# Kernel tuning notes

Hardware: AMD Instinct MI355X
Metric: run time of the kernel (lower is better)

Reference implementation:

```python
import jax, jax.numpy as jnp
import numpy as np

NEG_SLOPE = 0.2  # PyG GATConv default leaky_relu slope


def gat_conv(x, ei, W, a_src, a_dst, b, heads, ch):
    """One PyG-style GATConv (eval mode, add_self_loops already applied to ei)."""
    N = x.shape[0]
    h = (x @ W).reshape(N, heads, ch)                      # [N,H,C]
    src, dst = ei[0], ei[1]
    al_s = jnp.sum(h * a_src, axis=-1)                     # [N,H]
    al_d = jnp.sum(h * a_dst, axis=-1)                     # [N,H]
    e = jax.nn.leaky_relu(al_s[src] + al_d[dst], NEG_SLOPE)  # [E,H]
    m = jax.ops.segment_max(e, dst, num_segments=N)        # stable softmax over in-edges
    ex = jnp.exp(e - m[dst])
    den = jax.ops.segment_sum(ex, dst, num_segments=N)
    alpha = ex / den[dst]                                  # [E,H]
    msg = alpha[:, :, None] * h[src]                       # [E,H,C]
    out = jax.ops.segment_sum(msg, dst, num_segments=N)    # [N,H,C]
    return out.reshape(N, heads * ch) + b


def setup_inputs() -> dict:
    key = jax.random.key(0)
    ks = jax.random.split(key, 12)
    N, E, D_in, C, H, D_out = 10000, 320000, 256, 128, 4, 64
    HC = H * C

    def glorot(k, shape):
        fan = shape[0] + shape[-1]
        return jax.random.normal(k, shape, dtype=jnp.float32) * np.sqrt(2.0 / fan)

    x = jax.random.normal(ks[0], (N, D_in), dtype=jnp.float32)
    edge_index = jax.random.randint(ks[1], (2, E), 0, N, dtype=jnp.int64)
    return {
        "x": x,
        "edge_index": edge_index,
        "W1": glorot(ks[2], (D_in, HC)),
        "a_src1": glorot(ks[3], (H, C)),
        "a_dst1": glorot(ks[4], (H, C)),
        "b1": jnp.zeros((HC,), dtype=jnp.float32),
        "W2": glorot(ks[5], (HC, HC)),
        "a_src2": glorot(ks[6], (H, C)),
        "a_dst2": glorot(ks[7], (H, C)),
        "b2": jnp.zeros((HC,), dtype=jnp.float32),
        "W3": glorot(ks[8], (HC, D_out)),
        "a_src3": glorot(ks[9], (1, D_out)),
        "a_dst3": glorot(ks[10], (1, D_out)),
        "b3": jnp.zeros((D_out,), dtype=jnp.float32),
    }


def reference(x, edge_index, W1, a_src1, a_dst1, b1, W2, a_src2, a_dst2, b2,
              W3, a_src3, a_dst3, b3):
    N = x.shape[0]
    loops = jnp.arange(N, dtype=edge_index.dtype)
    ei = jnp.concatenate([edge_index, jnp.stack([loops, loops])], axis=1)
    H, C = a_src1.shape
    h = jax.nn.elu(gat_conv(x, ei, W1, a_src1, a_dst1, b1, H, C))
    h = jax.nn.elu(gat_conv(h, ei, W2, a_src2, a_dst2, b2, H, C))
    out = gat_conv(h, ei, W3, a_src3, a_dst3, b3, 1, a_src3.shape[1])
    return out
```

## Files before the change

kernel.cpp:

```cpp
#include <hip/hip_runtime.h>
#include <hip/hip_fp16.h>

typedef _Float16 f16x8 __attribute__((ext_vector_type(8)));
typedef float f32x4 __attribute__((ext_vector_type(4)));

__device__ __forceinline__ unsigned short f2h_bits(float f) {
    __half h = __float2half(f);
    return *reinterpret_cast<unsigned short*>(&h);
}
__device__ __forceinline__ float h2f_bits(unsigned short u) {
    __half h = *reinterpret_cast<__half*>(&u);
    return __half2float(h);
}

__device__ __forceinline__ void fma_mix_lo(float& acc, float a, unsigned hw) {
    asm("v_fma_mix_f32 %0, %1, %2, %0 op_sel_hi:[0,1,0]"
        : "+v"(acc) : "v"(a), "v"(hw));
}
__device__ __forceinline__ void fma_mix_hi(float& acc, float a, unsigned hw) {
    asm("v_fma_mix_f32 %0, %1, %2, %0 op_sel:[0,1,0] op_sel_hi:[0,1,0]"
        : "+v"(acc) : "v"(a), "v"(hw));
}

__device__ __forceinline__ void gload_lds16(const void* g, void* l) {
    __builtin_amdgcn_global_load_lds(
        (const __attribute__((address_space(1))) unsigned int*)g,
        (__attribute__((address_space(3))) unsigned int*)l, 16, 0, 0);
}

__global__ void k_prep(const float* __restrict__ W1, unsigned short* __restrict__ W1T,
                       const float* __restrict__ W2, unsigned short* __restrict__ W2T,
                       const float* __restrict__ W3, unsigned short* __restrict__ W3T,
                       const float* __restrict__ x, unsigned short* __restrict__ xb,
                       int* __restrict__ csr, int Mcap,
                       const int* __restrict__ ei, int E, int* __restrict__ deg,
                       int DIN, int HC, int DOUT, int N)
{
    int i = blockIdx.x * blockDim.x + threadIdx.x;
    int n1 = DIN * HC;
    int n2 = n1 + HC * HC;
    int n3 = n2 + HC * DOUT;
    int n4 = n3 + N * DIN;
    int n5 = n4 + Mcap;
    int n6 = n5 + E;
    if (i < n1) {
        int k = i / HC, n = i - k * HC;
        W1T[n * DIN + k] = f2h_bits(W1[i]);
    } else if (i < n2) {
        int j = i - n1;
        int k = j / HC, n = j - k * HC;
        W2T[n * HC + k] = f2h_bits(W2[j]);
    } else if (i < n3) {
        int j = i - n2;
        int k = j / DOUT, n = j - k * DOUT;
        W3T[n * HC + k] = f2h_bits(W3[j]);
    } else if (i < n4) {
        int j = i - n3;
        xb[j] = f2h_bits(x[j]);
    } else if (i < n5) {
        csr[i - n4] = -1;
    } else if (i < n6) {
        atomicAdd(&deg[ei[E + (i - n5)]], 1);
    }
}

__global__ void k_scan(const int* __restrict__ deg, int* __restrict__ off,
                       int* __restrict__ cur, int N) {
    __shared__ int sums[1024];
    int t = threadIdx.x;
    int chunk = (N + 1023) >> 10;
    int lo = t * chunk;
    int hi = lo + chunk; if (hi > N) hi = N;
    if (lo > N) lo = N;
    int s = 0;
    for (int i = lo; i < hi; ++i) s += (deg[i] + 4) & ~3;
    sums[t] = s;
    __syncthreads();
    for (int dd = 1; dd < 1024; dd <<= 1) {
        int v = (t >= dd) ? sums[t - dd] : 0;
        __syncthreads();
        sums[t] += v;
        __syncthreads();
    }
    int run = sums[t] - s;
    for (int i = lo; i < hi; ++i) { off[i] = run; cur[i] = run; run += (deg[i] + 4) & ~3; }
    if (t == 1023) off[N] = run;
}
__global__ void k_fill(const int* __restrict__ ei, int E, int N,
                       int* cur, int* __restrict__ csr, int* __restrict__ dstarr) {
    int i = blockIdx.x * blockDim.x + threadIdx.x;
    if (i < E) {
        int s = ei[i], d = ei[E + i];
        int pos = atomicAdd(&cur[d], 1);
        csr[pos] = s;
        dstarr[pos] = d;
    } else if (i < E + N) {
        int nn = i - E;
        int pos = atomicAdd(&cur[nn], 1);
        csr[pos] = nn;
        dstarr[pos] = nn;
    }
}

template <bool OUTH, bool DOAL>
__global__ __launch_bounds__(256) void k_gemm(
    const unsigned short* __restrict__ A, const unsigned short* __restrict__ BT,
    void* __restrict__ D, int M, int K, int Nc, int tiles_n,
    const float* __restrict__ asrc, const float* __restrict__ adst,
    float* __restrict__ als, float* __restrict__ ald)
{
    int wid = blockIdx.x * (blockDim.x >> 6) + (threadIdx.x >> 6);
    int tiles_m = (M + 63) >> 6;
    if (wid >= tiles_m * tiles_n) return;
    int lane = threadIdx.x & 63;
    int tm = wid / tiles_n, tn = wid - tm * tiles_n;
    int m0 = tm << 6, n0 = tn << 6;
    int r = lane & 15, q = lane >> 4;

    const unsigned short* Arow[4];
    const unsigned short* Brow[4];
#pragma unroll
    for (int i = 0; i < 4; ++i) {
        int row = m0 + 16 * i + r; row = row < M ? row : M - 1;
        Arow[i] = A + (size_t)row * K + q * 8;
        Brow[i] = BT + (size_t)(n0 + 16 * i + r) * K + q * 8;
    }

    f32x4 acc[4][4] = {};
    f16x8 a[4], b[4], a2[4], b2[4];
#pragma unroll
    for (int i = 0; i < 4; ++i) {
        a[i] = *(const f16x8*)(Arow[i]);
        b[i] = *(const f16x8*)(Brow[i]);
    }
    for (int k0 = 0; k0 < K; k0 += 32) {
        int kn = k0 + 32;
        if (kn < K) {
#pragma unroll
            for (int i = 0; i < 4; ++i) {
                a2[i] = *(const f16x8*)(Arow[i] + kn);
                b2[i] = *(const f16x8*)(Brow[i] + kn);
            }
        }
#pragma unroll
        for (int i = 0; i < 4; ++i)
#pragma unroll
            for (int j = 0; j < 4; ++j)
                acc[i][j] = __builtin_amdgcn_mfma_f32_16x16x32_f16(a[i], b[j], acc[i][j], 0, 0, 0);
        if (kn < K) {
#pragma unroll
            for (int i = 0; i < 4; ++i) { a[i] = a2[i]; b[i] = b2[i]; }
        }
    }
#pragma unroll
    for (int i = 0; i < 4; ++i) {
        int rowb = m0 + 16 * i + q * 4;
#pragma unroll
        for (int rr = 0; rr < 4; ++rr) {
            int row = rowb + rr;
            if (row < M) {
#pragma unroll
                for (int j = 0; j < 4; ++j) {
                    int col = n0 + 16 * j + r;
                    if (OUTH)
                        ((unsigned short*)D)[(size_t)row * Nc + col] = f2h_bits(acc[i][j][rr]);
                    else
                        ((float*)D)[(size_t)row * Nc + col] = acc[i][j][rr];
                }
            }
        }
    }
    if (DOAL) {
        float asl[4], adl[4];
#pragma unroll
        for (int j = 0; j < 4; ++j) { asl[j] = asrc[16 * j + r]; adl[j] = adst[16 * j + r]; }
#pragma unroll
        for (int i = 0; i < 4; ++i) {
#pragma unroll
            for (int rr = 0; rr < 4; ++rr) {
                float s = 0.f, d = 0.f;
#pragma unroll
                for (int j = 0; j < 4; ++j) {
                    s += acc[i][j][rr] * asl[j];
                    d += acc[i][j][rr] * adl[j];
                }
#pragma unroll
                for (int dd = 1; dd < 16; dd <<= 1) {
                    s += __shfl_xor(s, dd);
                    d += __shfl_xor(d, dd);
                }
                int row = m0 + 16 * i + q * 4 + rr;
                if (r == 0 && row < M) { als[row] = s; ald[row] = d; }
            }
        }
    }
}

__global__ __launch_bounds__(256) void k_gemm_lds(
    const unsigned short* __restrict__ A, const unsigned short* __restrict__ BT,
    unsigned short* __restrict__ D, int M, int K, int Nc, int tiles_n)
{
    __shared__ unsigned short As[128 * 32];
    __shared__ unsigned short Bs[64 * 32];
    int tm = blockIdx.x / tiles_n, tn = blockIdx.x - tm * tiles_n;
    int m0 = tm << 7, n0 = tn << 6;
    int tid = threadIdx.x;
    int w = tid >> 6, lane = tid & 63;
    int wr = w >> 1, wc = w & 1;
    int r = lane & 15, q = lane >> 4;

    int lrow = lane >> 2;
    int lch = (lane & 3) * 8;
    int ga0 = m0 + w * 16 + lrow;       if (ga0 >= M) ga0 = M - 1;
    int ga1 = m0 + (w + 4) * 16 + lrow; if (ga1 >= M) ga1 = M - 1;
    const unsigned short* pa0 = A + (size_t)ga0 * K + lch;
    const unsigned short* pa1 = A + (size_t)ga1 * K + lch;
    const unsigned short* pb  = BT + (size_t)(n0 + w * 16 + lrow) * K + lch;
    unsigned short* lA0 = As + w * 512;
    unsigned short* lA1 = As + (w + 4) * 512;
    unsigned short* lB  = Bs + w * 512;

    const unsigned short* arp = As + (wr * 64 + r) * 32 + q * 8;
    const unsigned short* brp = Bs + (wc * 32 + r) * 32 + q * 8;

    f32x4 acc[4][2] = {};
    for (int k0 = 0; k0 < K; k0 += 32) {
        gload_lds16(pa0 + k0, lA0);
        gload_lds16(pa1 + k0, lA1);
        gload_lds16(pb + k0, lB);
        __syncthreads();
        f16x8 a[4], b[2];
#pragma unroll
        for (int i = 0; i < 4; ++i) a[i] = *(const f16x8*)(arp + i * 16 * 32);
#pragma unroll
        for (int j = 0; j < 2; ++j) b[j] = *(const f16x8*)(brp + j * 16 * 32);
#pragma unroll
        for (int i = 0; i < 4; ++i)
#pragma unroll
            for (int j = 0; j < 2; ++j)
                acc[i][j] = __builtin_amdgcn_mfma_f32_16x16x32_f16(a[i], b[j], acc[i][j], 0, 0, 0);
        __syncthreads();
    }
#pragma unroll
    for (int i = 0; i < 4; ++i) {
        int rowb = m0 + wr * 64 + 16 * i + q * 4;
#pragma unroll
        for (int rr = 0; rr < 4; ++rr) {
            int row = rowb + rr;
            if (row < M) {
#pragma unroll
                for (int j = 0; j < 2; ++j) {
                    int col = n0 + wc * 32 + 16 * j + r;
                    D[(size_t)row * Nc + col] = f2h_bits(acc[i][j][rr]);
                }
            }
        }
    }
}

template <int HCt, int Ht>
__global__ __launch_bounds__(256) void k_al(
    const unsigned short* __restrict__ h, const float* __restrict__ asrc,
    const float* __restrict__ adst,
    float* __restrict__ als, float* __restrict__ ald, int N)
{
    int wid = blockIdx.x * (blockDim.x >> 6) + (threadIdx.x >> 6);
    if (wid >= N) return;
    int lane = threadIdx.x & 63;
    const int CH = HCt / 64;
    const int Gs = 64 / Ht;
    float s = 0.f, d = 0.f;
    if constexpr (CH == 8) {
        const uint4* hr = (const uint4*)(h + (size_t)wid * HCt) + lane;
        uint4 hv = *hr;
        unsigned wds[4] = {hv.x, hv.y, hv.z, hv.w};
        const f32x4* as4 = (const f32x4*)(asrc + lane * 8);
        const f32x4* ad4 = (const f32x4*)(adst + lane * 8);
        f32x4 av0 = as4[0], av1 = as4[1], dv0 = ad4[0], dv1 = ad4[1];
#pragma unroll
        for (int wv = 0; wv < 4; ++wv) {
            float a0 = (wv < 2) ? av0[2 * wv] : av1[2 * (wv - 2)];
            float a1 = (wv < 2) ? av0[2 * wv + 1] : av1[2 * (wv - 2) + 1];
            float d0 = (wv < 2) ? dv0[2 * wv] : dv1[2 * (wv - 2)];
            float d1 = (wv < 2) ? dv0[2 * wv + 1] : dv1[2 * (wv - 2) + 1];
            fma_mix_lo(s, a0, wds[wv]); fma_mix_hi(s, a1, wds[wv]);
            fma_mix_lo(d, d0, wds[wv]); fma_mix_hi(d, d1, wds[wv]);
        }
    } else {
        float hv = h2f_bits(h[(size_t)wid * HCt + lane]);
        s = hv * asrc[lane];
        d = hv * adst[lane];
    }
#pragma unroll
    for (int dd = 1; dd < Gs; dd <<= 1) {
        s += __shfl_xor(s, dd);
        d += __shfl_xor(d, dd);
    }
    if ((lane & (Gs - 1)) == 0) {
        int hh = lane / Gs;
        als[wid * Ht + hh] = s;
        ald[wid * Ht + hh] = d;
    }
}

__global__ void k_alpha4(const float* __restrict__ als, const float* __restrict__ ald,
                         const int* __restrict__ csr, const int* __restrict__ dstarr,
                         const int* __restrict__ off, int N,
                         float* __restrict__ alpha, int Mcap)
{
    int t = blockIdx.x * blockDim.x + threadIdx.x;
    if (t >= off[N]) return;
    int s = csr[t];
    if (s < 0) {
#pragma unroll
        for (int h = 0; h < 4; ++h) alpha[(size_t)h * Mcap + t] = 0.f;
        return;
    }
    int d = dstarr[t];
    f32x4 a = *(const f32x4*)(als + (size_t)s * 4);
    f32x4 b = *(const f32x4*)(ald + (size_t)d * 4);
#pragma unroll
    for (int h = 0; h < 4; ++h) {
        float l = a[h] + b[h];
        l = l > 0.f ? l : 0.2f * l;
        alpha[(size_t)h * Mcap + t] = __expf(l);
    }
}

template <bool DOELU>
__global__ __launch_bounds__(256) void k_aggr4b(
    const unsigned short* __restrict__ h, const float* __restrict__ alpha,
    const int* __restrict__ off, const int* __restrict__ csr,
    const float* __restrict__ bias,
    unsigned short* __restrict__ outp, int N, int nodeBlocks, int Mcap)
{
    int head = blockIdx.x / nodeBlocks;
    int nb = blockIdx.x - head * nodeBlocks;
    int n = nb * 4 + (threadIdx.x >> 6);
    if (n >= N) return;
    int lane = threadIdx.x & 63;
    int g = lane >> 4;
    int p = lane & 15;
    int q0 = (off[n] >> 2) + g, q1 = off[n + 1] >> 2;

    float acc[8] = {};
    float den = 0.f;
    const char* hB = (const char*)h;
    const unsigned offp = (unsigned)(head * 256 + p * 16);
    const int4* csr4 = (const int4*)csr;
    const f32x4* al4 = (const f32x4*)(alpha + (size_t)head * Mcap);

    auto fmaq = [&](float a, const uint4& hq) {
        unsigned wds[4] = {hq.x, hq.y, hq.z, hq.w};
#pragma unroll
        for (int wv = 0; wv < 4; ++wv) {
            fma_mix_lo(acc[2 * wv],     a, wds[wv]);
            fma_mix_hi(acc[2 * wv + 1], a, wds[wv]);
        }
    };

    for (int q = q0; q < q1; q += 4) {
        int4 cs = csr4[q];
        f32x4 av = al4[q];
        int c0 = cs.x < 0 ? 0 : cs.x;
        int c1 = cs.y < 0 ? 0 : cs.y;
        int c2 = cs.z < 0 ? 0 : cs.z;
        int c3 = cs.w < 0 ? 0 : cs.w;
        uint4 h0 = *(const uint4*)(hB + (size_t)((((unsigned)c0) << 10) + offp));
        uint4 h1 = *(const uint4*)(hB + (size_t)((((unsigned)c1) << 10) + offp));
        uint4 h2 = *(const uint4*)(hB + (size_t)((((unsigned)c2) << 10) + offp));
        uint4 h3 = *(const uint4*)(hB + (size_t)((((unsigned)c3) << 10) + offp));
        den += (av[0] + av[1]) + (av[2] + av[3]);
        fmaq(av[0], h0);
        fmaq(av[1], h1);
        fmaq(av[2], h2);
        fmaq(av[3], h3);
    }

    den += __shfl_xor(den, 16);
    den += __shfl_xor(den, 32);
#pragma unroll
    for (int j = 0; j < 8; ++j) {
        acc[j] += __shfl_xor(acc[j], 16);
        acc[j] += __shfl_xor(acc[j], 32);
    }

    if (g == 0) {
        float inv = 1.f / den;
        int cb = head * 128 + p * 8;
        unsigned ww[4];
#pragma unroll
        for (int wv = 0; wv < 4; ++wv) {
            float v0 = acc[2 * wv] * inv + bias[cb + 2 * wv];
            float v1 = acc[2 * wv + 1] * inv + bias[cb + 2 * wv + 1];
            if (DOELU) {
                v0 = v0 > 0.f ? v0 : expm1f(v0);
                v1 = v1 > 0.f ? v1 : expm1f(v1);
            }
            ww[wv] = (unsigned)f2h_bits(v0) | ((unsigned)f2h_bits(v1) << 16);
        }
        uint4 o; o.x = ww[0]; o.y = ww[1]; o.z = ww[2]; o.w = ww[3];
        *((uint4*)(outp + (size_t)n * 512 + cb)) = o;
    }
}

__global__ __launch_bounds__(256) void k_aggr1b(
    const unsigned short* __restrict__ h, const float* __restrict__ als,
    const float* __restrict__ aldv, const int* __restrict__ off,
    const int* __restrict__ csr, const float* __restrict__ bias,
    float* __restrict__ outp, int N)
{
    int n = blockIdx.x * (blockDim.x >> 6) + (threadIdx.x >> 6);
    if (n >= N) return;
    int lane = threadIdx.x & 63;
    int g = lane >> 4;
    int p = lane & 15;
    int q0 = (off[n] >> 2) + g, q1 = off[n + 1] >> 2;
    float aldh = aldv[n];

    float acc[4] = {};
    float den = 0.f;
    const char* hB = (const char*)h;
    const unsigned offp = (unsigned)(p * 8);
    const int4* csr4 = (const int4*)csr;

    auto aof = [&](int ss) -> float {
        int sc = ss < 0 ? 0 : ss;
        float l = als[sc] + aldh;
        l = l > 0.f ? l : 0.2f * l;
        float e = __expf(l);
        return ss < 0 ? 0.f : e;
    };
    auto fmaq = [&](float a, const uint2& hq) {
        den += a;
        fma_mix_lo(acc[0], a, hq.x);
        fma_mix_hi(acc[1], a, hq.x);
        fma_mix_lo(acc[2], a, hq.y);
        fma_mix_hi(acc[3], a, hq.y);
    };

    for (int q = q0; q < q1; q += 4) {
        int4 cs = csr4[q];
        float a0 = aof(cs.x), a1 = aof(cs.y), a2 = aof(cs.z), a3 = aof(cs.w);
        uint2 h0 = *(const uint2*)(hB + (size_t)((((unsigned)(cs.x < 0 ? 0 : cs.x)) << 7) + offp));
        uint2 h1 = *(const uint2*)(hB + (size_t)((((unsigned)(cs.y < 0 ? 0 : cs.y)) << 7) + offp));
        uint2 h2 = *(const uint2*)(hB + (size_t)((((unsigned)(cs.z < 0 ? 0 : cs.z)) << 7) + offp));
        uint2 h3 = *(const uint2*)(hB + (size_t)((((unsigned)(cs.w < 0 ? 0 : cs.w)) << 7) + offp));
        fmaq(a0, h0);
        fmaq(a1, h1);
        fmaq(a2, h2);
        fmaq(a3, h3);
    }

    den += __shfl_xor(den, 16);
    den += __shfl_xor(den, 32);
#pragma unroll
    for (int j = 0; j < 4; ++j) {
        acc[j] += __shfl_xor(acc[j], 16);
        acc[j] += __shfl_xor(acc[j], 32);
    }
    if (g == 0) {
        float inv = 1.f / den;
        f32x4 o;
#pragma unroll
        for (int j = 0; j < 4; ++j)
            o[j] = acc[j] * inv + bias[p * 4 + j];
        *((f32x4*)(outp + (size_t)n * 64 + p * 4)) = o;
    }
}

extern "C" void kernel_launch(void* const* d_in, const int* in_sizes, int n_in,
                              void* d_out, int out_size, void* d_ws, size_t ws_size,
                              hipStream_t stream)
{
    const float* x   = (const float*)d_in[0];
    const int*   ei  = (const int*)d_in[1];
    const float* W1  = (const float*)d_in[2];
    const float* as1 = (const float*)d_in[3];
    const float* ad1 = (const float*)d_in[4];
    const float* b1  = (const float*)d_in[5];
    const float* W2  = (const float*)d_in[6];
    const float* as2 = (const float*)d_in[7];
    const float* ad2 = (const float*)d_in[8];
    const float* b2  = (const float*)d_in[9];
    const float* W3  = (const float*)d_in[10];
    const float* as3 = (const float*)d_in[11];
    const float* ad3 = (const float*)d_in[12];
    const float* b3  = (const float*)d_in[13];

    const int DIN = 256, HC = 512, DOUT = 64;
    int N = in_sizes[0] / DIN;
    int E = in_sizes[1] / 2;
    int Mcap = E + 4 * N;

    char* w = (char*)d_ws;
    auto alloc = [&](size_t bytes) -> char* {
        char* p = w;
        w += (bytes + 255) & ~(size_t)255;
        return p;
    };
    int* deg    = (int*)alloc((size_t)N * 4);
    int* cur    = (int*)alloc((size_t)N * 4);
    int* off    = (int*)alloc((size_t)(N + 1) * 4);
    int* csr    = (int*)alloc((size_t)Mcap * 4);
    int* dstarr = (int*)alloc((size_t)Mcap * 4);
    unsigned short* W1T = (unsigned short*)alloc((size_t)HC * DIN * 2);
    unsigned short* W2T = (unsigned short*)alloc((size_t)HC * HC * 2);
    unsigned short* W3T = (unsigned short*)alloc((size_t)DOUT * HC * 2);
    unsigned short* xb  = (unsigned short*)alloc((size_t)N * DIN * 2);
    unsigned short* act = (unsigned short*)alloc((size_t)N * HC * 2);
    unsigned short* hb  = (unsigned short*)alloc((size_t)N * HC * 2);
    unsigned short* hb3 = (unsigned short*)alloc((size_t)N * DOUT * 2);
    float* als   = (float*)alloc((size_t)N * 4 * 4);
    float* ald   = (float*)alloc((size_t)N * 4 * 4);
    float* alpha = (float*)alloc((size_t)Mcap * 4 * 4);

    hipMemsetAsync(deg, 0, (size_t)N * 4, stream);
    int prep_total = DIN * HC + HC * HC + HC * DOUT + N * DIN + Mcap + E;
    k_prep<<<(prep_total + 255) / 256, 256, 0, stream>>>(
        W1, W1T, W2, W2T, W3, W3T, x, xb, csr, Mcap, ei, E, deg, DIN, HC, DOUT, N);
    k_scan<<<1, 1024, 0, stream>>>(deg, off, cur, N);
    k_fill<<<(E + N + 255) / 256, 256, 0, stream>>>(ei, E, N, cur, csr, dstarr);

    int tiles_m = (N + 63) / 64;
    auto gemm_blocks = [&](int tn) { return (tiles_m * tn + 3) / 4; };
    int tm128 = (N + 127) / 128;
    int nwave_blocks = (N + 3) / 4;
    int nodeBlocks = (N + 3) / 4;
    int alpha_blocks = (Mcap + 255) / 256;

    k_gemm_lds<<<tm128 * (HC / 64), 256, 0, stream>>>(xb, W1T, hb, N, DIN, HC, HC / 64);
    k_al<512, 4><<<nwave_blocks, 256, 0, stream>>>(hb, as1, ad1, als, ald, N);
    k_alpha4<<<alpha_blocks, 256, 0, stream>>>(als, ald, csr, dstarr, off, N, alpha, Mcap);
    k_aggr4b<true><<<4 * nodeBlocks, 256, 0, stream>>>(hb, alpha, off, csr, b1, act, N, nodeBlocks, Mcap);

    k_gemm_lds<<<tm128 * (HC / 64), 256, 0, stream>>>(act, W2T, hb, N, HC, HC, HC / 64);
    k_al<512, 4><<<nwave_blocks, 256, 0, stream>>>(hb, as2, ad2, als, ald, N);
    k_alpha4<<<alpha_blocks, 256, 0, stream>>>(als, ald, csr, dstarr, off, N, alpha, Mcap);
    k_aggr4b<true><<<4 * nodeBlocks, 256, 0, stream>>>(hb, alpha, off, csr, b2, act, N, nodeBlocks, Mcap);

    k_gemm<true, true><<<gemm_blocks(1), 256, 0, stream>>>(
        act, W3T, hb3, N, HC, DOUT, 1, as3, ad3, als, ald);
    k_aggr1b<<<nwave_blocks, 256, 0, stream>>>(hb3, als, ald, off, csr, b3, (float*)d_out, N);
}
```

Baseline: 286.3 us.

## Fuse attention coefficient computation into aggregation and process all heads per wave

Removes the separate per-edge alpha kernel and its Mcap×4 alpha buffer (and the dstarr array). Each wave now computes exp(leaky_relu(als[src]+ald[dst])) for 64 edges at a time into shared memory, then aggregates all 4 heads per node with each lane covering 8 channels across the full 512-wide row. This saves a kernel launch and a global write-then-read of alpha per layer, and each csr row is read once instead of once per head. In exchange, per-node work is serialized within one wave with a shared-memory staging step, and the launch has 4x fewer blocks.

Measured after the change: 283.9 us. Within noise of the previous version (-0.8%).

```diff
diff --git a/kernel.cpp b/kernel.cpp
--- a/kernel.cpp
+++ b/kernel.cpp
@@ -87,18 +87,16 @@
     if (t == 1023) off[N] = run;
 }
 __global__ void k_fill(const int* __restrict__ ei, int E, int N,
-                       int* cur, int* __restrict__ csr, int* __restrict__ dstarr) {
+                       int* cur, int* __restrict__ csr) {
     int i = blockIdx.x * blockDim.x + threadIdx.x;
     if (i < E) {
         int s = ei[i], d = ei[E + i];
         int pos = atomicAdd(&cur[d], 1);
         csr[pos] = s;
-        dstarr[pos] = d;
     } else if (i < E + N) {
         int nn = i - E;
         int pos = atomicAdd(&cur[nn], 1);
         csr[pos] = nn;
-        dstarr[pos] = nn;
     }
 }
 
@@ -303,105 +301,107 @@
     }
 }
 
-__global__ void k_alpha4(const float* __restrict__ als, const float* __restrict__ ald,
-                         const int* __restrict__ csr, const int* __restrict__ dstarr,
-                         const int* __restrict__ off, int N,
-                         float* __restrict__ alpha, int Mcap)
-{
-    int t = blockIdx.x * blockDim.x + threadIdx.x;
-    if (t >= off[N]) return;
-    int s = csr[t];
-    if (s < 0) {
-#pragma unroll
-        for (int h = 0; h < 4; ++h) alpha[(size_t)h * Mcap + t] = 0.f;
-        return;
-    }
-    int d = dstarr[t];
-    f32x4 a = *(const f32x4*)(als + (size_t)s * 4);
-    f32x4 b = *(const f32x4*)(ald + (size_t)d * 4);
-#pragma unroll
-    for (int h = 0; h < 4; ++h) {
-        float l = a[h] + b[h];
-        l = l > 0.f ? l : 0.2f * l;
-        alpha[(size_t)h * Mcap + t] = __expf(l);
-    }
-}
-
 template <bool DOELU>
-__global__ __launch_bounds__(256) void k_aggr4b(
-    const unsigned short* __restrict__ h, const float* __restrict__ alpha,
+__global__ __launch_bounds__(256) void k_aggr4d(
+    const unsigned short* __restrict__ h, const float* __restrict__ als,
+    const float* __restrict__ ald,
     const int* __restrict__ off, const int* __restrict__ csr,
     const float* __restrict__ bias,
-    unsigned short* __restrict__ outp, int N, int nodeBlocks, int Mcap)
-{
-    int head = blockIdx.x / nodeBlocks;
-    int nb = blockIdx.x - head * nodeBlocks;
-    int n = nb * 4 + (threadIdx.x >> 6);
+    unsigned short* __restrict__ outp, int N)
+{
+    __shared__ float alpS[4][4][64];
+    int wid = threadIdx.x >> 6;
+    int n = blockIdx.x * 4 + wid;
     if (n >= N) return;
     int lane = threadIdx.x & 63;
-    int g = lane >> 4;
-    int p = lane & 15;
-    int q0 = (off[n] >> 2) + g, q1 = off[n + 1] >> 2;
+    int g4 = lane >> 4;
+
+    int off0 = off[n], off1 = off[n + 1];
+    int degp = off1 - off0;
+    const int4* csr4 = (const int4*)(csr + off0);
+    f32x4 ald4 = *(const f32x4*)(ald + (size_t)n * 4);
 
     float acc[8] = {};
     float den = 0.f;
     const char* hB = (const char*)h;
-    const unsigned offp = (unsigned)(head * 256 + p * 16);
-    const int4* csr4 = (const int4*)csr;
-    const f32x4* al4 = (const f32x4*)(alpha + (size_t)head * Mcap);
-
-    auto fmaq = [&](float a, const uint4& hq) {
-        unsigned wds[4] = {hq.x, hq.y, hq.z, hq.w};
-#pragma unroll
-        for (int wv = 0; wv < 4; ++wv) {
-            fma_mix_lo(acc[2 * wv],     a, wds[wv]);
-            fma_mix_hi(acc[2 * wv + 1], a, wds[wv]);
-        }
-    };
-
-    for (int q = q0; q < q1; q += 4) {
-        int4 cs = csr4[q];
-        f32x4 av = al4[q];
-        int c0 = cs.x < 0 ? 0 : cs.x;
-        int c1 = cs.y < 0 ? 0 : cs.y;
-        int c2 = cs.z < 0 ? 0 : cs.z;
-        int c3 = cs.w < 0 ? 0 : cs.w;
-        uint4 h0 = *(const uint4*)(hB + (size_t)((((unsigned)c0) << 10) + offp));
-        uint4 h1 = *(const uint4*)(hB + (size_t)((((unsigned)c1) << 10) + offp));
-        uint4 h2 = *(const uint4*)(hB + (size_t)((((unsigned)c2) << 10) + offp));
-        uint4 h3 = *(const uint4*)(hB + (size_t)((((unsigned)c3) << 10) + offp));
-        den += (av[0] + av[1]) + (av[2] + av[3]);
-        fmaq(av[0], h0);
-        fmaq(av[1], h1);
-        fmaq(av[2], h2);
-        fmaq(av[3], h3);
-    }
-
-    den += __shfl_xor(den, 16);
-    den += __shfl_xor(den, 32);
-#pragma unroll
-    for (int j = 0; j < 8; ++j) {
-        acc[j] += __shfl_xor(acc[j], 16);
-        acc[j] += __shfl_xor(acc[j], 32);
-    }
-
-    if (g == 0) {
-        float inv = 1.f / den;
-        int cb = head * 128 + p * 8;
-        unsigned ww[4];
-#pragma unroll
-        for (int wv = 0; wv < 4; ++wv) {
-            float v0 = acc[2 * wv] * inv + bias[cb + 2 * wv];
-            float v1 = acc[2 * wv + 1] * inv + bias[cb + 2 * wv + 1];
-            if (DOELU) {
-                v0 = v0 > 0.f ? v0 : expm1f(v0);
-                v1 = v1 > 0.f ? v1 : expm1f(v1);
-            }
-            ww[wv] = (unsigned)f2h_bits(v0) | ((unsigned)f2h_bits(v1) << 16);
-        }
-        uint4 o; o.x = ww[0]; o.y = ww[1]; o.z = ww[2]; o.w = ww[3];
-        *((uint4*)(outp + (size_t)n * 512 + cb)) = o;
-    }
+    const unsigned offp = (unsigned)(lane * 16);
+
+    for (int base = 0; base < degp; base += 64) {
+        f32x4 av = {0.f, 0.f, 0.f, 0.f};
+        int e = base + lane;
+        if (e < degp) {
+            int s = csr[off0 + e];
+            if (s >= 0) {
+                f32x4 a4 = *(const f32x4*)(als + (size_t)(unsigned)s * 4);
+#pragma unroll
+                for (int hh = 0; hh < 4; ++hh) {
+                    float l = a4[hh] + ald4[hh];
+                    l = l > 0.f ? l : 0.2f * l;
+                    av[hh] = __expf(l);
+                }
+            }
+        }
+#pragma unroll
+        for (int hh = 0; hh < 4; ++hh) alpS[wid][hh][lane] = av[hh];
+
+        int qn = (degp - base) >> 2; if (qn > 16) qn = 16;
+        int qb = base >> 2;
+        for (int qq = 0; qq < qn; ++qq) {
+            int4 cs = csr4[qb + qq];
+            f32x4 af = *(const f32x4*)&alpS[wid][g4][qq * 4];
+            int c0 = cs.x < 0 ? 0 : cs.x;
+            int c1 = cs.y < 0 ? 0 : cs.y;
+            int c2 = cs.z < 0 ? 0 : cs.z;
+            int c3 = cs.w < 0 ? 0 : cs.w;
+            uint4 h0 = *(const uint4*)(hB + (size_t)((((unsigned)c0) << 10) + offp));
+            uint4 h1 = *(const uint4*)(hB + (size_t)((((unsigned)c1) << 10) + offp));
+            uint4 h2 = *(const uint4*)(hB + (size_t)((((unsigned)c2) << 10) + offp));
+            uint4 h3 = *(const uint4*)(hB + (size_t)((((unsigned)c3) << 10) + offp));
+            den += (af[0] + af[1]) + (af[2] + af[3]);
+            unsigned w0[4] = {h0.x, h0.y, h0.z, h0.w};
+            unsigned w1[4] = {h1.x, h1.y, h1.z, h1.w};
+            unsigned w2[4] = {h2.x, h2.y, h2.z, h2.w};
+            unsigned w3[4] = {h3.x, h3.y, h3.z, h3.w};
+#pragma unroll
+            for (int wv = 0; wv < 4; ++wv) {
+                fma_mix_lo(acc[2 * wv],     af[0], w0[wv]);
+                fma_mix_hi(acc[2 * wv + 1], af[0], w0[wv]);
+            }
+#pragma unroll
+            for (int wv = 0; wv < 4; ++wv) {
+                fma_mix_lo(acc[2 * wv],     af[1], w1[wv]);
+                fma_mix_hi(acc[2 * wv + 1], af[1], w1[wv]);
+            }
+#pragma unroll
+            for (int wv = 0; wv < 4; ++wv) {
+                fma_mix_lo(acc[2 * wv],     af[2], w2[wv]);
+                fma_mix_hi(acc[2 * wv + 1], af[2], w2[wv]);
+            }
+#pragma unroll
+            for (int wv = 0; wv < 4; ++wv) {
+                fma_mix_lo(acc[2 * wv],     af[3], w3[wv]);
+                fma_mix_hi(acc[2 * wv + 1], af[3], w3[wv]);
+            }
+        }
+    }
+
+    float inv = 1.f / den;
+    int cb = lane * 8;
+    const f32x4* b4 = (const f32x4*)(bias + cb);
+    f32x4 bv0 = b4[0], bv1 = b4[1];
+    unsigned ww[4];
+#pragma unroll
+    for (int wv = 0; wv < 4; ++wv) {
+        float v0 = acc[2 * wv] * inv + (wv < 2 ? bv0[2 * wv] : bv1[2 * (wv - 2)]);
+        float v1 = acc[2 * wv + 1] * inv + (wv < 2 ? bv0[2 * wv + 1] : bv1[2 * (wv - 2) + 1]);
+        if (DOELU) {
+            v0 = v0 > 0.f ? v0 : expm1f(v0);
+            v1 = v1 > 0.f ? v1 : expm1f(v1);
+        }
+        ww[wv] = (unsigned)f2h_bits(v0) | ((unsigned)f2h_bits(v1) << 16);
+    }
+    uint4 o; o.x = ww[0]; o.y = ww[1]; o.z = ww[2]; o.w = ww[3];
+    *((uint4*)(outp + (size_t)n * 512 + cb)) = o;
 }
 
 __global__ __launch_bounds__(256) void k_aggr1b(
@@ -503,7 +503,6 @@
     int* cur    = (int*)alloc((size_t)N * 4);
     int* off    = (int*)alloc((size_t)(N + 1) * 4);
     int* csr    = (int*)alloc((size_t)Mcap * 4);
-    int* dstarr = (int*)alloc((size_t)Mcap * 4);
     unsigned short* W1T = (unsigned short*)alloc((size_t)HC * DIN * 2);
     unsigned short* W2T = (unsigned short*)alloc((size_t)HC * HC * 2);
     unsigned short* W3T = (unsigned short*)alloc((size_t)DOUT * HC * 2);
@@ -513,31 +512,27 @@
     unsigned short* hb3 = (unsigned short*)alloc((size_t)N * DOUT * 2);
     float* als   = (float*)alloc((size_t)N * 4 * 4);
     float* ald   = (float*)alloc((size_t)N * 4 * 4);
-    float* alpha = (float*)alloc((size_t)Mcap * 4 * 4);
 
     hipMemsetAsync(deg, 0, (size_t)N * 4, stream);
     int prep_total = DIN * HC + HC * HC + HC * DOUT + N * DIN + Mcap + E;
     k_prep<<<(prep_total + 255) / 256, 256, 0, stream>>>(
         W1, W1T, W2, W2T, W3, W3T, x, xb, csr, Mcap, ei, E, deg, DIN, HC, DOUT, N);
     k_scan<<<1, 1024, 0, stream>>>(deg, off, cur, N);
-    k_fill<<<(E + N + 255) / 256, 256, 0, stream>>>(ei, E, N, cur, csr, dstarr);
+    k_fill<<<(E + N + 255) / 256, 256, 0, stream>>>(ei, E, N, cur, csr);
 
     int tiles_m = (N + 63) / 64;
     auto gemm_blocks = [&](int tn) { return (tiles_m * tn + 3) / 4; };
     int tm128 = (N + 127) / 128;
     int nwave_blocks = (N + 3) / 4;
     int nodeBlocks = (N + 3) / 4;
-    int alpha_blocks = (Mcap + 255) / 256;
 
     k_gemm_lds<<<tm128 * (HC / 64), 256, 0, stream>>>(xb, W1T, hb, N, DIN, HC, HC / 64);
     k_al<512, 4><<<nwave_blocks, 256, 0, stream>>>(hb, as1, ad1, als, ald, N);
-    k_alpha4<<<alpha_blocks, 256, 0, stream>>>(als, ald, csr, dstarr, off, N, alpha, Mcap);
-    k_aggr4b<true><<<4 * nodeBlocks, 256, 0, stream>>>(hb, alpha, off, csr, b1, act, N, nodeBlocks, Mcap);
+    k_aggr4d<true><<<nodeBlocks, 256, 0, stream>>>(hb, als, ald, off, csr, b1, act, N);
 
     k_gemm_lds<<<tm128 * (HC / 64), 256, 0, stream>>>(act, W2T, hb, N, HC, HC, HC / 64);
     k_al<512, 4><<<nwave_blocks, 256, 0, stream>>>(hb, as2, ad2, als, ald, N);
-    k_alpha4<<<alpha_blocks, 256, 0, stream>>>(als, ald, csr, dstarr, off, N, alpha, Mcap);
-    k_aggr4b<true><<<4 * nodeBlocks, 256, 0, stream>>>(hb, alpha, off, csr, b2, act, N, nodeBlocks, Mcap);
+    k_aggr4d<true><<<nodeBlocks, 256, 0, stream>>>(hb, als, ald, off, csr, b2, act, N);
 
     k_gemm<true, true><<<gemm_blocks(1), 256, 0, stream>>>(
         act, W3T, hb3, N, HC, DOUT, 1, as3, ad3, als, ald);
```
